# Kernel optimization log

Measured on AMD Instinct MI355X. Metric: run time of the kernel, lower is better.

The kernel has to match this reference:

```python
import jax, jax.numpy as jnp
import numpy as np

N_CLASSES = 80
TOPK = 13
ALPHA = 1.0
BETA = 6.0
EPS = 1e-9
BS, N_ANCHORS, N_MAX = 32, 8400, 100


def setup_inputs() -> dict:
    key = jax.random.key(0)
    k1, k2, k3, k4, k5, k6 = jax.random.split(key, 6)
    pred_scores = jax.random.uniform(k1, (BS, N_ANCHORS, N_CLASSES), dtype=jnp.float32)
    anchor_points = jax.random.uniform(k2, (N_ANCHORS, 2), dtype=jnp.float32) * 640.0
    # predicted boxes centered on anchor points (valid xyxy)
    wh = jax.random.uniform(k3, (BS, N_ANCHORS, 2), dtype=jnp.float32) * 100.0 + 4.0
    ctr = anchor_points[None]
    pred_bboxes = jnp.concatenate([ctr - wh / 2, ctr + wh / 2], axis=-1)
    gt_lt = jax.random.uniform(k4, (BS, N_MAX, 2), dtype=jnp.float32) * 500.0
    gt_wh = jax.random.uniform(k5, (BS, N_MAX, 2), dtype=jnp.float32) * 120.0 + 8.0
    gt_bboxes = jnp.concatenate([gt_lt, gt_lt + gt_wh], axis=-1)
    gt_labels = jax.random.randint(k6, (BS, N_MAX, 1), 0, N_CLASSES).astype(jnp.int32)
    mask_gt = jnp.ones((BS, N_MAX, 1), dtype=jnp.float32)
    return {"pred_scores": pred_scores, "pred_bboxes": pred_bboxes,
            "anchor_points": anchor_points, "gt_labels": gt_labels,
            "gt_bboxes": gt_bboxes, "mask_gt": mask_gt}


def _batch_iou(a, b):
    # a: [bs, n, 4], b: [bs, m, 4] (xyxy) -> [bs, n, m]
    lt = jnp.maximum(a[:, :, None, :2], b[:, None, :, :2])
    rb = jnp.minimum(a[:, :, None, 2:], b[:, None, :, 2:])
    wh = jnp.clip(rb - lt, 0.0)
    inter = wh[..., 0] * wh[..., 1]
    area_a = ((a[..., 2] - a[..., 0]) * (a[..., 3] - a[..., 1]))[:, :, None]
    area_b = ((b[..., 2] - b[..., 0]) * (b[..., 3] - b[..., 1]))[:, None, :]
    return inter / (area_a + area_b - inter + EPS)


def _assign(pred_scores, pred_bboxes, anchor_points, gt_labels, gt_bboxes, mask_gt):
    bs, n_anchors, n_classes = pred_scores.shape
    n_max = gt_bboxes.shape[1]
    labels = gt_labels[..., 0].astype(jnp.int32)  # [bs, n_max]

    # alignment metric: bbox_scores[b,g,a] = pred_scores[b,a,labels[b,g]]
    ps_t = jnp.swapaxes(pred_scores, 1, 2)  # [bs, C, n_anchors]
    bbox_scores = jnp.take_along_axis(ps_t, labels[:, :, None], axis=1)  # [bs, n_max, n_anchors]
    overlaps = _batch_iou(gt_bboxes, pred_bboxes)  # [bs, n_max, n_anchors]
    align_metric = jnp.power(bbox_scores, ALPHA) * jnp.power(overlaps, BETA)

    # anchor centers inside gt boxes
    ap = anchor_points[None, None, :, :]  # [1,1,n_anchors,2]
    deltas = jnp.concatenate(
        [ap - gt_bboxes[:, :, None, :2], gt_bboxes[:, :, None, 2:] - ap], axis=-1)
    is_in_gts = (deltas.min(axis=-1) > EPS).astype(align_metric.dtype)  # [bs,n_max,n_anchors]

    # topk candidate selection
    metrics = align_metric * is_in_gts
    _, topk_idxs = jax.lax.top_k(metrics, TOPK)  # [bs, n_max, TOPK]
    topk_mask = (mask_gt > 0)  # [bs, n_max, 1], broadcasts over TOPK
    topk_idxs = jnp.where(topk_mask, topk_idxs, 0)

    def count_row(idx):  # idx: [TOPK] -> anchor hit counts [n_anchors]
        return jnp.zeros((n_anchors,), jnp.int32).at[idx].add(1)
    counts = jax.vmap(jax.vmap(count_row))(topk_idxs)  # [bs, n_max, n_anchors]
    is_in_topk = jnp.where(counts > 1, 0, counts).astype(metrics.dtype)

    mask_pos = is_in_topk * is_in_gts * mask_gt  # [bs, n_max, n_anchors]

    # fix collisions: anchors assigned to multiple GTs keep the max-IoU GT
    mask_pos_sum = mask_pos.sum(axis=1)  # [bs, n_anchors]
    multi = mask_pos_sum[:, None, :] > 1
    is_max_overlaps = jax.nn.one_hot(overlaps.argmax(axis=1), n_max, axis=1,
                                     dtype=mask_pos.dtype)  # [bs, n_max, n_anchors]
    mask_pos = jnp.where(multi, is_max_overlaps, mask_pos)
    mask_pos_sum = mask_pos.sum(axis=1)
    assigned_gt_idx = mask_pos.argmax(axis=1)  # [bs, n_anchors]

    # final assignments via flattened gather
    flat_idx = assigned_gt_idx + jnp.arange(bs, dtype=jnp.int32)[:, None] * n_max
    assigned_labels = labels.reshape(-1)[flat_idx]  # [bs, n_anchors]
    assigned_bboxes = gt_bboxes.reshape(-1, 4)[flat_idx]  # [bs, n_anchors, 4]
    assigned_labels = jnp.where(assigned_labels < 0, 0, assigned_labels)
    assigned_scores = jax.nn.one_hot(assigned_labels, n_classes, dtype=pred_scores.dtype)
    pos = mask_pos_sum > 0
    assigned_scores = jnp.where(pos[..., None], assigned_scores, 0.0)
    assigned_labels = jnp.where(pos, assigned_labels, n_classes)

    # normalize scores by alignment metric
    align_metric = align_metric * mask_pos
    pos_align = align_metric.max(axis=-1, keepdims=True)  # [bs, n_max, 1]
    pos_overlaps = (overlaps * mask_pos).max(axis=-1, keepdims=True)
    norm = (align_metric * pos_overlaps / (pos_align + EPS)).max(axis=1)[..., None]  # [bs,n_anchors,1]
    assigned_scores = assigned_scores * norm

    return assigned_labels, assigned_bboxes, assigned_scores, pos


def reference(pred_scores, pred_bboxes, anchor_points, gt_labels, gt_bboxes, mask_gt):
    return _assign(pred_scores, pred_bboxes, anchor_points, gt_labels, gt_bboxes, mask_gt)
```

## Files before the change

### kernel.cpp

```cpp
#include <hip/hip_runtime.h>

#define BS 32
#define NA 8400
#define NMAX 100
#define NC 80
#define TOPK 13
#define EPSF 1e-9f
#define WCAP 1024
#define NSTRIP 64
#define STRIP_INV 0.1f

#define OFF_LBL  0
#define OFF_BOX  (BS*NA)
#define OFF_SCR  (BS*NA + BS*NA*4)
#define OFF_POS  (BS*NA + BS*NA*4 + BS*NA*NC)

#define NROWS (BS*NMAX)
#define NSC4  (BS*NA*NC/4)
#define ZBLK  120

__global__ __launch_bounds__(1024) void bin_zero_kernel(
    const float* __restrict__ anchor_points,
    int* __restrict__ strip_off, float4* __restrict__ sAPI,
    unsigned int* __restrict__ pz_base,
    unsigned int* __restrict__ pcount,
    float* __restrict__ out)
{
    int t = threadIdx.x;
    if (blockIdx.x != 0) {
        int zb = blockIdx.x - 1;
        if (zb == 0) {
            uint4* pz = (uint4*)pz_base;
            uint4 zz = make_uint4(0u, 0u, 0u, 0u);
            for (int i = t; i < 1600; i += 1024) pz[i] = zz;
            if (t == 0) *pcount = 0u;
        }
        float4* sz = (float4*)(out + OFF_SCR);
        float4 zf = make_float4(0.f, 0.f, 0.f, 0.f);
        for (int i = zb * 1024 + t; i < NSC4; i += ZBLK * 1024) sz[i] = zf;
        return;
    }

    __shared__ int cnt[NSTRIP];
    __shared__ int cur[NSTRIP];
    if (t < NSTRIP) cnt[t] = 0;
    __syncthreads();
    const float2* ap2 = (const float2*)anchor_points;
    for (int a = t; a < NA; a += 1024) {
        int s = (int)(ap2[a].y * STRIP_INV);
        s = s < 0 ? 0 : (s > NSTRIP - 1 ? NSTRIP - 1 : s);
        atomicAdd(&cnt[s], 1);
    }
    __syncthreads();
    if (t < 64) {
        int v = cnt[t];
        int inc = v;
        #pragma unroll
        for (int d = 1; d < 64; d <<= 1) {
            int o = __shfl_up(inc, d, 64);
            if (t >= d) inc += o;
        }
        int excl = inc - v;
        cur[t] = excl; strip_off[t] = excl;
        if (t == 63) strip_off[64] = inc;
    }
    __syncthreads();
    for (int a = t; a < NA; a += 1024) {
        float2 p = ap2[a];
        int s = (int)(p.y * STRIP_INV);
        s = s < 0 ? 0 : (s > NSTRIP - 1 ? NSTRIP - 1 : s);
        int pos = atomicAdd(&cur[s], 1);
        sAPI[pos] = make_float4(p.x, p.y, __int_as_float(a), 0.f);
    }
}

__global__ __launch_bounds__(256) void topk_kernel(
    const float* __restrict__ pred_scores,
    const float* __restrict__ pred_bboxes,
    const int*   __restrict__ gt_labels,
    const float* __restrict__ gt_bboxes,
    const float* __restrict__ mask_gt,
    const int*   __restrict__ strip_off,
    const float4* __restrict__ sAPI,
    unsigned int*   __restrict__ ccount,
    unsigned short* __restrict__ clist)
{
    __shared__ unsigned short aidx[4][WCAP];
    int t = threadIdx.x;
    int wave = t >> 6;
    int lane = t & 63;
    int row = blockIdx.x * 4 + wave;
    if (mask_gt[row] <= 0.f) {
        if (lane == 0) ccount[row] = 0u;
        return;
    }
    int b = row / NMAX;

    const float* gbp = gt_bboxes + (size_t)row * 4;
    float gx1 = gbp[0], gy1 = gbp[1], gx2 = gbp[2], gy2 = gbp[3];
    int lab = gt_labels[row];

    int s_lo = (int)(gy1 * STRIP_INV); s_lo = s_lo < 0 ? 0 : (s_lo > NSTRIP-1 ? NSTRIP-1 : s_lo);
    int s_hi = (int)(gy2 * STRIP_INV); s_hi = s_hi < 0 ? 0 : (s_hi > NSTRIP-1 ? NSTRIP-1 : s_hi);
    int lo = strip_off[s_lo], hi = strip_off[s_hi + 1];

    int cnt = 0;
    for (int base = lo; base < hi; base += 64) {
        int p = base + lane;
        bool hit = false; int a = 0;
        if (p < hi) {
            float4 ap = sAPI[p];
            a = __float_as_int(ap.z);
            hit = (ap.x - gx1 > EPSF) && (ap.y - gy1 > EPSF) &&
                  (gx2 - ap.x > EPSF) && (gy2 - ap.y > EPSF);
        }
        unsigned long long mb = __ballot(hit);
        if (hit) {
            int my = cnt + __popcll(mb & ((1ULL << lane) - 1ULL));
            if (my < WCAP) aidx[wave][my] = (unsigned short)a;
        }
        cnt += __popcll(mb);
    }
    if (cnt > WCAP) cnt = WCAP;

    unsigned long long loc[TOPK];
    #pragma unroll
    for (int i = 0; i < TOPK; i++) loc[i] = 0ULL;
    const float4* pb4 = (const float4*)pred_bboxes;
    for (int p = lane; p < cnt; p += 64) {
        int a = aidx[wave][p];
        float4 pb = pb4[b * NA + a];
        float s = pred_scores[((size_t)b * NA + a) * NC + lab];
        float lx = fmaxf(gx1, pb.x), ly = fmaxf(gy1, pb.y);
        float rx = fminf(gx2, pb.z), ry = fminf(gy2, pb.w);
        float w = fmaxf(rx - lx, 0.f), h = fmaxf(ry - ly, 0.f);
        float inter = w * h;
        float aa = (gx2 - gx1) * (gy2 - gy1);
        float ab = (pb.z - pb.x) * (pb.w - pb.y);
        float iou = inter / (aa + ab - inter + EPSF);
        float i2 = iou * iou;
        float m = s * (i2 * i2 * i2);
        if (m > 0.f) {
            unsigned long long key =
                ((unsigned long long)__float_as_uint(m) << 32) |
                (unsigned int)(NA - a);
            #pragma unroll
            for (int i = 0; i < TOPK; i++) {
                if (key > loc[i]) { unsigned long long tmp = loc[i]; loc[i] = key; key = tmp; }
            }
        }
    }

    int picks = TOPK;
    for (int r = 0; r < TOPK; r++) {
        unsigned long long h = loc[0];
        unsigned long long m = h;
        #pragma unroll
        for (int s = 32; s > 0; s >>= 1) {
            unsigned long long o = __shfl_xor(m, s, 64);
            m = o > m ? o : m;
        }
        if (m == 0ULL) { picks = r; break; }
        unsigned long long ball = __ballot(h == m);
        if (lane == (int)__builtin_ctzll(ball)) {
            #pragma unroll
            for (int i = 0; i < TOPK - 1; i++) loc[i] = loc[i + 1];
            loc[TOPK - 1] = 0ULL;
            int a = NA - (int)(unsigned int)(m & 0xFFFFFFFFULL);
            clist[row * TOPK + r] = (unsigned short)a;
        }
    }
    if (lane == 0) ccount[row] = (unsigned int)picks;
}

__global__ __launch_bounds__(256) void resolve_kernel(
    const float* __restrict__ pred_scores,
    const float* __restrict__ pred_bboxes,
    const int*   __restrict__ gt_labels,
    const float* __restrict__ gt_bboxes,
    const unsigned int*   __restrict__ ccount,
    const unsigned short* __restrict__ clist,
    unsigned int* __restrict__ pa_bits, unsigned int* __restrict__ po_bits,
    unsigned int* __restrict__ pcount, uint4* __restrict__ plist,
    float* __restrict__ out)
{
    __shared__ float4 gtb[NMAX];
    __shared__ int    glab[NMAX];
    __shared__ int    ccnt[NMAX];
    __shared__ unsigned int pkl[256];
    int b = blockIdx.y;
    int t = threadIdx.x;
    if (t < NMAX) {
        gtb[t]  = ((const float4*)gt_bboxes)[b * NMAX + t];
        glab[t] = gt_labels[b * NMAX + t];
        ccnt[t] = (int)ccount[b * NMAX + t];
    }
    pkl[t] = 0u;
    __syncthreads();

    int lo = blockIdx.x * 256;
    for (int e = t; e < NMAX * TOPK; e += 256) {
        int j = e / TOPK, k = e - j * TOPK;
        if (k < ccnt[j]) {
            int a = clist[(b * NMAX + j) * TOPK + k];
            unsigned int w = (unsigned int)(a - lo);
            if (w < 256u) atomicAdd(&pkl[w], (1u << 16) | (unsigned int)j);
        }
    }
    __syncthreads();

    int ai = lo + t;
    bool valid = ai < NA;
    int idx = b * NA + (valid ? ai : 0);
    unsigned int pk = valid ? pkl[t] : 0u;

    int js = -1; float align = 0.f; int lab = 0;
    if (pk != 0u) {
        float4 pb = ((const float4*)pred_bboxes)[idx];
        float iou;
        if ((pk >> 16) == 1u) {
            js = (int)(pk & 0xFFFFu);
            float4 g = gtb[js];
            float lx = fmaxf(g.x, pb.x), ly = fmaxf(g.y, pb.y);
            float rx = fminf(g.z, pb.z), ry = fminf(g.w, pb.w);
            float w = fmaxf(rx - lx, 0.f), h = fmaxf(ry - ly, 0.f);
            float inter = w * h;
            float aa = (g.z - g.x) * (g.w - g.y);
            float ab = (pb.z - pb.x) * (pb.w - pb.y);
            iou = inter / (aa + ab - inter + EPSF);
        } else {
            float best = -1.f; js = 0;
            for (int j = 0; j < NMAX; j++) {
                float4 g = gtb[j];
                float lx = fmaxf(g.x, pb.x), ly = fmaxf(g.y, pb.y);
                float rx = fminf(g.z, pb.z), ry = fminf(g.w, pb.w);
                float w = fmaxf(rx - lx, 0.f), h = fmaxf(ry - ly, 0.f);
                float inter = w * h;
                float aa = (g.z - g.x) * (g.w - g.y);
                float ab = (pb.z - pb.x) * (pb.w - pb.y);
                float v = inter / (aa + ab - inter + EPSF);
                if (v > best) { best = v; js = j; }
            }
            iou = best;
        }
        lab = glab[js];
        float s = pred_scores[(size_t)idx * NC + lab];
        float i2 = iou * iou;
        align = s * (i2 * i2 * i2);
        atomicMax(&pa_bits[b * NMAX + js], __float_as_uint(align));
        atomicMax(&po_bits[b * NMAX + js], __float_as_uint(iou));
    }

    if (valid) {
        bool pos = js >= 0;
        int j0 = pos ? js : 0;
        int albl = pos ? lab : glab[0];
        out[OFF_LBL + idx] = pos ? (float)albl : (float)NC;
        ((float4*)(out + OFF_BOX))[idx] = gtb[j0];
        out[OFF_POS + idx] = pos ? 1.f : 0.f;
    }

    bool pos = valid && js >= 0;
    unsigned long long mb = __ballot(pos);
    int n = __popcll(mb);
    if (n > 0) {
        int lane = t & 63;
        int leader = (int)__builtin_ctzll(mb);
        unsigned int base = 0;
        if (lane == leader) base = atomicAdd(pcount, (unsigned int)n);
        base = (unsigned int)__shfl((int)base, leader, 64);
        if (pos) {
            unsigned int myoff = (unsigned int)__popcll(mb & ((1ULL << (t & 63)) - 1ULL));
            plist[base + myoff] = make_uint4((unsigned int)idx,
                                             (unsigned int)(b * NMAX + js),
                                             __float_as_uint(align),
                                             (unsigned int)lab);
        }
    }
}

__global__ __launch_bounds__(256) void scatter_kernel(
    const unsigned int* __restrict__ pcount, const uint4* __restrict__ plist,
    const unsigned int* __restrict__ pa_bits, const unsigned int* __restrict__ po_bits,
    float* __restrict__ out)
{
    int n = (int)*pcount;
    for (int i = blockIdx.x * 256 + threadIdx.x; i < n; i += 64 * 256) {
        uint4 e = plist[i];
        float pa = __uint_as_float(pa_bits[e.y]);
        float po = __uint_as_float(po_bits[e.y]);
        float norm = __uint_as_float(e.z) * po / (pa + EPSF);
        out[OFF_SCR + (size_t)e.x * NC + e.w] = norm;
    }
}

extern "C" void kernel_launch(void* const* d_in, const int* in_sizes, int n_in,
                              void* d_out, int out_size, void* d_ws, size_t ws_size,
                              hipStream_t stream) {
    const float* pred_scores   = (const float*)d_in[0];
    const float* pred_bboxes   = (const float*)d_in[1];
    const float* anchor_points = (const float*)d_in[2];
    const int*   gt_labels     = (const int*)d_in[3];
    const float* gt_bboxes     = (const float*)d_in[4];
    const float* mask_gt       = (const float*)d_in[5];

    char* ws = (char*)d_ws;
    unsigned int*   pa_bits = (unsigned int*)(ws);
    unsigned int*   po_bits = (unsigned int*)(ws + 12800);
    unsigned int*   ccount  = (unsigned int*)(ws + 25600);
    unsigned short* clist   = (unsigned short*)(ws + 38400);
    int*    strip_off = (int*)(ws + 121600);
    float4* sAPI      = (float4*)(ws + 122112);
    unsigned int* pcount = (unsigned int*)(ws + 256512);
    uint4*  plist     = (uint4*)(ws + 256528);

    float* out = (float*)d_out;

    bin_zero_kernel<<<1 + ZBLK, 1024, 0, stream>>>(
        anchor_points, strip_off, sAPI, pa_bits, pcount, out);

    topk_kernel<<<NROWS / 4, 256, 0, stream>>>(
        pred_scores, pred_bboxes, gt_labels, gt_bboxes, mask_gt,
        strip_off, sAPI, ccount, clist);

    dim3 rgrid((NA + 255) / 256, BS);
    resolve_kernel<<<rgrid, 256, 0, stream>>>(
        pred_scores, pred_bboxes, gt_labels, gt_bboxes, ccount, clist,
        pa_bits, po_bits, pcount, plist, out);

    scatter_kernel<<<64, 256, 0, stream>>>(pcount, plist, pa_bits, po_bits, out);
}
```

Measured before the change: 245.6 us.

## Resolve multi-GT anchors with wave-cooperative argmax and prefetch pred boxes

```diff
diff --git a/kernel.cpp b/kernel.cpp
--- a/kernel.cpp
+++ b/kernel.cpp
@@ -17,7 +17,7 @@
 
 #define NROWS (BS*NMAX)
 #define NSC4  (BS*NA*NC/4)
-#define ZBLK  120
+#define ZBLK  511
 
 __global__ __launch_bounds__(1024) void bin_zero_kernel(
     const float* __restrict__ anchor_points,
@@ -190,6 +190,14 @@
     __shared__ unsigned int pkl[256];
     int b = blockIdx.y;
     int t = threadIdx.x;
+    int lane = t & 63;
+    int lo = blockIdx.x * 256;
+    int ai = lo + t;
+    bool valid = ai < NA;
+    int idx = b * NA + (valid ? ai : 0);
+
+    float4 pb = ((const float4*)pred_bboxes)[idx];
+
     if (t < NMAX) {
         gtb[t]  = ((const float4*)gt_bboxes)[b * NMAX + t];
         glab[t] = gt_labels[b * NMAX + t];
@@ -198,7 +206,6 @@
     pkl[t] = 0u;
     __syncthreads();
 
-    int lo = blockIdx.x * 256;
     for (int e = t; e < NMAX * TOPK; e += 256) {
         int j = e / TOPK, k = e - j * TOPK;
         if (k < ccnt[j]) {
@@ -209,40 +216,59 @@
     }
     __syncthreads();
 
-    int ai = lo + t;
-    bool valid = ai < NA;
-    int idx = b * NA + (valid ? ai : 0);
     unsigned int pk = valid ? pkl[t] : 0u;
-
-    int js = -1; float align = 0.f; int lab = 0;
-    if (pk != 0u) {
-        float4 pb = ((const float4*)pred_bboxes)[idx];
-        float iou;
-        if ((pk >> 16) == 1u) {
-            js = (int)(pk & 0xFFFFu);
-            float4 g = gtb[js];
-            float lx = fmaxf(g.x, pb.x), ly = fmaxf(g.y, pb.y);
-            float rx = fminf(g.z, pb.z), ry = fminf(g.w, pb.w);
-            float w = fmaxf(rx - lx, 0.f), h = fmaxf(ry - ly, 0.f);
-            float inter = w * h;
-            float aa = (g.z - g.x) * (g.w - g.y);
-            float ab = (pb.z - pb.x) * (pb.w - pb.y);
-            iou = inter / (aa + ab - inter + EPSF);
-        } else {
-            float best = -1.f; js = 0;
-            for (int j = 0; j < NMAX; j++) {
+    int js = -1; float iou = 0.f;
+
+    if ((pk >> 16) == 1u) {
+        js = (int)(pk & 0xFFFFu);
+        float4 g = gtb[js];
+        float lx = fmaxf(g.x, pb.x), ly = fmaxf(g.y, pb.y);
+        float rx = fminf(g.z, pb.z), ry = fminf(g.w, pb.w);
+        float w = fmaxf(rx - lx, 0.f), h = fmaxf(ry - ly, 0.f);
+        float inter = w * h;
+        float aa = (g.z - g.x) * (g.w - g.y);
+        float ab = (pb.z - pb.x) * (pb.w - pb.y);
+        iou = inter / (aa + ab - inter + EPSF);
+    }
+
+    unsigned long long mm = __ballot((pk >> 16) > 1u);
+    while (mm) {
+        int src = (int)__builtin_ctzll(mm);
+        mm &= mm - 1ULL;
+        float qx1 = __shfl(pb.x, src, 64), qy1 = __shfl(pb.y, src, 64);
+        float qx2 = __shfl(pb.z, src, 64), qy2 = __shfl(pb.w, src, 64);
+        float qab = (qx2 - qx1) * (qy2 - qy1);
+        unsigned long long bestkey = 0ULL;
+        #pragma unroll
+        for (int rep = 0; rep < 2; rep++) {
+            int j = lane + rep * 64;
+            if (j < NMAX) {
                 float4 g = gtb[j];
-                float lx = fmaxf(g.x, pb.x), ly = fmaxf(g.y, pb.y);
-                float rx = fminf(g.z, pb.z), ry = fminf(g.w, pb.w);
+                float lx = fmaxf(g.x, qx1), ly = fmaxf(g.y, qy1);
+                float rx = fminf(g.z, qx2), ry = fminf(g.w, qy2);
                 float w = fmaxf(rx - lx, 0.f), h = fmaxf(ry - ly, 0.f);
                 float inter = w * h;
                 float aa = (g.z - g.x) * (g.w - g.y);
-                float ab = (pb.z - pb.x) * (pb.w - pb.y);
-                float v = inter / (aa + ab - inter + EPSF);
-                if (v > best) { best = v; js = j; }
+                float v = inter / (aa + qab - inter + EPSF);
+                unsigned long long key =
+                    ((unsigned long long)__float_as_uint(v) << 32) |
+                    (unsigned int)(NMAX - 1 - j);
+                if (key > bestkey) bestkey = key;
             }
-            iou = best;
-        }
+        }
+        #pragma unroll
+        for (int s = 32; s > 0; s >>= 1) {
+            unsigned long long o = __shfl_xor(bestkey, s, 64);
+            bestkey = o > bestkey ? o : bestkey;
+        }
+        if (lane == src) {
+            js  = NMAX - 1 - (int)(unsigned int)(bestkey & 0xFFFFFFFFULL);
+            iou = __uint_as_float((unsigned int)(bestkey >> 32));
+        }
+    }
+
+    float align = 0.f; int lab = 0;
+    if (js >= 0) {
         lab = glab[js];
         float s = pred_scores[(size_t)idx * NC + lab];
         float i2 = iou * iou;
@@ -254,8 +280,7 @@
     if (valid) {
         bool pos = js >= 0;
         int j0 = pos ? js : 0;
-        int albl = pos ? lab : glab[0];
-        out[OFF_LBL + idx] = pos ? (float)albl : (float)NC;
+        out[OFF_LBL + idx] = pos ? (float)glab[j0] : (float)NC;
         ((float4*)(out + OFF_BOX))[idx] = gtb[j0];
         out[OFF_POS + idx] = pos ? 1.f : 0.f;
     }
@@ -264,13 +289,12 @@
     unsigned long long mb = __ballot(pos);
     int n = __popcll(mb);
     if (n > 0) {
-        int lane = t & 63;
         int leader = (int)__builtin_ctzll(mb);
         unsigned int base = 0;
         if (lane == leader) base = atomicAdd(pcount, (unsigned int)n);
         base = (unsigned int)__shfl((int)base, leader, 64);
         if (pos) {
-            unsigned int myoff = (unsigned int)__popcll(mb & ((1ULL << (t & 63)) - 1ULL));
+            unsigned int myoff = (unsigned int)__popcll(mb & ((1ULL << lane) - 1ULL));
             plist[base + myoff] = make_uint4((unsigned int)idx,
                                              (unsigned int)(b * NMAX + js),
                                              __float_as_uint(align),
```

Result: no change. 244.8 us (-0.3%).
